# Optimization experiments

Measured on AMD Instinct MI355X. Metric: run time of the kernel, lower is better.

## Reference

```python
import jax, jax.numpy as jnp
import numpy as np


def crf_log_likelihood(logits, tags, mask, transitions, start_trans, end_trans):
    """AllenNLP-style linear-chain CRF log-likelihood, summed over the batch.
    logits: [B,T,K] float, tags: [B,T] int, mask: [B,T] float (1=valid).
    include_start_end_transitions=True.
    """
    B, T, K = logits.shape
    lt = jnp.transpose(logits, (1, 0, 2))          # [T,B,K]
    mt = jnp.transpose(mask, (1, 0))               # [T,B]
    tt = jnp.transpose(tags, (1, 0))               # [T,B]

    # ---- partition function (forward algorithm) ----
    alpha0 = start_trans + lt[0]                   # [B,K]

    def part_step(alpha, xs):
        emit, m = xs                               # emit [B,K], m [B]
        # inner[b,i,j] = alpha[b,i] + transitions[i,j] + emit[b,j]
        inner = alpha[:, :, None] + emit[:, None, :] + transitions[None, :, :]
        new_alpha = jax.nn.logsumexp(inner, axis=1)
        alpha = new_alpha * m[:, None] + alpha * (1.0 - m[:, None])
        return alpha, None

    alpha, _ = jax.lax.scan(part_step, alpha0, (lt[1:], mt[1:]))
    log_denominator = jax.nn.logsumexp(alpha + end_trans, axis=1)  # [B]

    # ---- joint (gold-path) score ----
    score0 = start_trans[tt[0]]                    # [B]

    def joint_step(score, xs):
        cur, nxt, emit, m_cur, m_nxt = xs
        trans_s = transitions[cur, nxt]                                   # [B]
        emit_s = jnp.take_along_axis(emit, cur[:, None], axis=1)[:, 0]    # [B]
        return score + trans_s * m_nxt + emit_s * m_cur, None

    score, _ = jax.lax.scan(joint_step, score0,
                            (tt[:-1], tt[1:], lt[:-1], mt[:-1], mt[1:]))
    last_idx = (jnp.sum(mt, axis=0) - 1.0).astype(jnp.int32)              # [B]
    last_tags = tt[last_idx, jnp.arange(B)]                               # [B]
    last_emit = jnp.take_along_axis(lt[-1], last_tags[:, None], axis=1)[:, 0]
    score = score + end_trans[last_tags] + last_emit * mt[-1]
    return jnp.sum(score - log_denominator)


def setup_inputs() -> dict:
    key = jax.random.key(0)
    ks = jax.random.split(key, 6)
    B, T, D, K = 64, 512, 768, 21
    vectors = jax.random.normal(ks[0], (B, T, D), dtype=jnp.float32)
    targets = jax.random.randint(ks[1], (B, T), 0, K, dtype=jnp.int32)
    mask = jnp.ones((B, T), dtype=jnp.int32)
    # Linear(input_dim, n_classes)
    W = jax.random.normal(ks[2], (K, D), dtype=jnp.float32) * (1.0 / np.sqrt(D))
    b = jax.random.normal(ks[3], (K,), dtype=jnp.float32) * 0.01
    transitions = jax.random.normal(ks[4], (K, K), dtype=jnp.float32) * 0.1
    se = jax.random.normal(ks[5], (2, K), dtype=jnp.float32) * 0.1
    return {"vectors": vectors, "targets": targets, "mask": mask,
            "W": W, "b": b, "transitions": transitions,
            "start_trans": se[0], "end_trans": se[1]}


def reference(vectors, targets, mask, W, b, transitions, start_trans, end_trans):
    logits = jnp.einsum('btd,kd->btk', vectors, W) + b     # proj
    maskf = mask.astype(logits.dtype)
    ll = crf_log_likelihood(logits, targets, maskf, transitions, start_trans, end_trans)
    loss = -ll / jnp.sum(maskf)
    return loss, logits
```

## Files before the change

### kernel.cpp

```cpp
#include <hip/hip_runtime.h>

#define B_ 64
#define T_ 512
#define D_ 768
#define K_ 21
#define NCHUNK 32
#define CLEN 16
#define GSTRIDE 448
#define LOG21 3.0445224377234229965f
#define WSTRIDE 776

using f16x8 = __attribute__((ext_vector_type(8))) _Float16;
using h16x4 = __attribute__((ext_vector_type(4))) _Float16;
using f32x4 = __attribute__((ext_vector_type(4))) float;

__global__ __launch_bounds__(256, 4) void proj_kernel(
    const float* __restrict__ A,
    const float* __restrict__ W,
    const float* __restrict__ bias,
    float* __restrict__ out)
{
    __shared__ _Float16 Wh[K_ * WSTRIDE];
    const int tid  = threadIdx.x;
    const int lane = tid & 63;
    const int w    = tid >> 6;
    const int m    = lane & 15;
    const int quad = lane >> 4;
    const int gw   = blockIdx.x * 4 + w;
    const float* Arow = A + ((size_t)gw * 16 + m) * D_;

    float4 pf[8];
    #pragma unroll
    for (int j = 0; j < 8; ++j) {
        const int s = j >> 1;
        const int off = s * 32 + quad * 8 + (j & 1) * 4;
        pf[j] = *(const float4*)(Arow + off);
    }

    {
        const float4* Wg = (const float4*)W;
        for (int i = tid; i < K_ * D_ / 4; i += 256) {
            const float4 v = Wg[i];
            const int fi = i * 4;
            const int r = fi / D_;
            const int c = fi - r * D_;
            h16x4 h;
            h[0] = (_Float16)v.x; h[1] = (_Float16)v.y;
            h[2] = (_Float16)v.z; h[3] = (_Float16)v.w;
            *(h16x4*)(&Wh[r * WSTRIDE + c]) = h;
        }
    }
    __syncthreads();

    f32x4 acc0 = {0.f, 0.f, 0.f, 0.f};
    f32x4 acc1 = {0.f, 0.f, 0.f, 0.f};
    const int n1 = (16 + m < K_) ? 16 + m : K_ - 1;

    for (int kt = 0; kt < 6; ++kt) {
        f16x8 af[4];
        #pragma unroll
        for (int s = 0; s < 4; ++s) {
            const float4 v0 = pf[2 * s], v1 = pf[2 * s + 1];
            f16x8 a;
            a[0] = (_Float16)v0.x; a[1] = (_Float16)v0.y;
            a[2] = (_Float16)v0.z; a[3] = (_Float16)v0.w;
            a[4] = (_Float16)v1.x; a[5] = (_Float16)v1.y;
            a[6] = (_Float16)v1.z; a[7] = (_Float16)v1.w;
            af[s] = a;
        }
        if (kt < 5) {
            const float* An = Arow + (kt + 1) * 128;
            #pragma unroll
            for (int j = 0; j < 8; ++j) {
                const int s = j >> 1;
                const int off = s * 32 + quad * 8 + (j & 1) * 4;
                pf[j] = *(const float4*)(An + off);
            }
        }
        #pragma unroll
        for (int s = 0; s < 4; ++s) {
            const f16x8 bf = *(const f16x8*)(&Wh[m  * WSTRIDE + kt * 128 + s * 32 + quad * 8]);
            const f16x8 cf = *(const f16x8*)(&Wh[n1 * WSTRIDE + kt * 128 + s * 32 + quad * 8]);
            acc0 = __builtin_amdgcn_mfma_f32_16x16x32_f16(af[s], bf, acc0, 0, 0, 0);
            acc1 = __builtin_amdgcn_mfma_f32_16x16x32_f16(af[s], cf, acc1, 0, 0, 0);
        }
    }

    const size_t rbase = (size_t)gw * 16 + quad * 4;
    {
        const float bb = bias[m];
        float* o = out + 1 + rbase * K_ + m;
        #pragma unroll
        for (int r = 0; r < 4; ++r) o[(size_t)r * K_] = acc0[r] + bb;
    }
    const int col2 = 16 + m;
    if (col2 < K_) {
        const float bb = bias[col2];
        float* o = out + 1 + rbase * K_ + col2;
        #pragma unroll
        for (int r = 0; r < 4; ++r) o[(size_t)r * K_] = acc1[r] + bb;
    }
}

__global__ __launch_bounds__(64, 1) void chunk_kernel(
    const float* __restrict__ outF,
    const int*   __restrict__ mask,
    const float* __restrict__ trans,
    float* __restrict__ G,
    float* __restrict__ SC,
    int*   __restrict__ cnt)
{
    __shared__ float M0[441], M1[441];
    __shared__ float sET[441];
    __shared__ float em[CLEN * K_];
    __shared__ float smx[CLEN];
    __shared__ int   smask[CLEN];

    const int c = blockIdx.x;
    const int b = blockIdx.y;
    const int lane = threadIdx.x;
    if (c == 0 && b == 0 && lane == 0) *cnt = 0;
    const int t0 = c * CLEN + 1;
    const int nst = min(CLEN, T_ - t0);
    const int i_ = lane / 3;
    const int jg = lane - i_ * 3;
    const bool act = lane < 63;

    const float* lg = outF + 1 + (size_t)b * T_ * K_;
    for (int idx = lane; idx < nst * K_; idx += 64) em[idx] = lg[t0 * K_ + idx];
    if (lane < nst) smask[lane] = mask[b * T_ + t0 + lane];
    for (int idx = lane; idx < 441; idx += 64) {
        M0[idx] = (idx % 22 == 0) ? 1.0f : 0.0f;
        sET[idx] = __expf(trans[idx]);
    }
    __syncthreads();

    if (lane < nst) {
        float mx = -1e30f;
        for (int j = 0; j < K_; ++j) mx = fmaxf(mx, em[lane * K_ + j]);
        smx[lane] = mx;
    }
    __syncthreads();
    for (int idx = lane; idx < nst * K_; idx += 64)
        em[idx] = __expf(em[idx] - smx[idx / K_]) * (1.0f / 21.0f);

    float ETc[K_ * 7];
    if (act) {
        #pragma unroll
        for (int mm = 0; mm < K_; ++mm) {
            #pragma unroll
            for (int q = 0; q < 7; ++q)
                ETc[mm * 7 + q] = sET[mm * K_ + jg * 7 + q];
        }
    }
    __syncthreads();

    int cur = 0;
    for (int s = 0; s < nst; ++s) {
        if (smask[s] != 0) {
            const float* Mr = cur ? M1 : M0;
            float*       Mw = cur ? M0 : M1;
            float facc[7] = {0.f,0.f,0.f,0.f,0.f,0.f,0.f};
            if (act) {
                #pragma unroll
                for (int mm = 0; mm < K_; ++mm) {
                    const float lm = Mr[i_ * K_ + mm];
                    #pragma unroll
                    for (int q = 0; q < 7; ++q)
                        facc[q] = fmaf(lm, ETc[mm * 7 + q], facc[q]);
                }
            }
            __syncthreads();
            if (act) {
                #pragma unroll
                for (int q = 0; q < 7; ++q)
                    Mw[i_ * K_ + jg * 7 + q] = facc[q] * em[s * K_ + jg * 7 + q];
            }
            __syncthreads();
            cur ^= 1;
        }
    }

    float* Gc = G + (size_t)(b * NCHUNK + c) * GSTRIDE;
    const float* Mf = cur ? M1 : M0;
    for (int idx = lane; idx < 441; idx += 64) Gc[idx] = Mf[idx];
    if (lane == 0) {
        float sc = 0.0f;
        for (int s = 0; s < nst; ++s)
            if (smask[s] != 0) sc += smx[s] + LOG21;
        SC[b * NCHUNK + c] = sc;
    }
}

__global__ __launch_bounds__(256) void scan_fin_kernel(
    const float* __restrict__ outF,
    const int*   __restrict__ tags,
    const int*   __restrict__ mask,
    const float* __restrict__ trans,
    const float* __restrict__ startT,
    const float* __restrict__ endT,
    const float* __restrict__ G,
    const float* __restrict__ SC,
    float* __restrict__ ll,
    float* __restrict__ msum,
    int*   __restrict__ cnt,
    float* __restrict__ outW)
{
    __shared__ float sG[NCHUNK * GSTRIDE];
    __shared__ float sm[T_];
    __shared__ int   st[T_];
    __shared__ float part[8];
    __shared__ int   lastF;
    const int tid = threadIdx.x;
    const int lane = tid & 63;
    const int w = tid >> 6;
    const int b = blockIdx.x;
    const float* lg = outF + 1 + (size_t)b * T_ * K_;

    {
        const float4* Gf4 = (const float4*)(G + (size_t)b * NCHUNK * GSTRIDE);
        float4* dst = (float4*)sG;
        for (int i = tid; i < NCHUNK * GSTRIDE / 4; i += 256) dst[i] = Gf4[i];
    }
    for (int t = tid; t < T_; t += 256) {
        sm[t] = (float)mask[b * T_ + t];
        st[t] = tags[b * T_ + t];
    }
    __syncthreads();

    float logZ = 0.0f;
    if (w == 0) {
        const float scv = (lane < NCHUNK) ? SC[b * NCHUNK + lane] : 0.0f;
        const int jc = min(lane, K_ - 1);
        float v = (lane < K_) ? __expf(startT[lane] + lg[lane]) : 0.0f;
        float C = 0.0f;
        for (int c = 0; c < NCHUNK; ++c) {
            const float* Gc = sG + c * GSTRIDE;
            float a0 = 0.f, a1 = 0.f, a2 = 0.f;
            #pragma unroll
            for (int i = 0; i < K_; i += 3) {
                a0 = fmaf(__shfl(v, i,     64), Gc[i * K_ + jc],       a0);
                a1 = fmaf(__shfl(v, i + 1, 64), Gc[(i + 1) * K_ + jc], a1);
                a2 = fmaf(__shfl(v, i + 2, 64), Gc[(i + 2) * K_ + jc], a2);
            }
            const float s = a0 + a1 + a2;
            const float s0 = __shfl(s, 0, 64);
            v = s / s0;
            C += __logf(s0) + __shfl(scv, c, 64);
        }
        float term = (lane < K_) ? v * __expf(endT[lane]) : 0.0f;
        #pragma unroll
        for (int off = 16; off >= 1; off >>= 1) term += __shfl_xor(term, off, 64);
        term += __shfl_xor(term, 32, 64);
        logZ = C + __logf(term);
    } else {
        float sc = 0.0f, ms = 0.0f;
        for (int t = tid - 64; t < T_; t += 192) {
            const float mt = sm[t];
            ms += mt;
            if (t < T_ - 1) {
                const int ct = st[t], nt2 = st[t + 1];
                sc += trans[ct * K_ + nt2] * sm[t + 1] + lg[t * K_ + ct] * mt;
            }
        }
        #pragma unroll
        for (int off = 32; off >= 1; off >>= 1) {
            sc += __shfl_xor(sc, off, 64);
            ms += __shfl_xor(ms, off, 64);
        }
        if (lane == 0) { part[w] = sc; part[4 + w] = ms; }
    }
    __syncthreads();

    if (tid == 0) {
        float sc = part[1] + part[2] + part[3];
        float ms = part[5] + part[6] + part[7];
        const int lastIdx = (int)ms - 1;
        const int lastTag = st[lastIdx];
        sc += startT[st[0]] + endT[lastTag] + lg[(T_ - 1) * K_ + lastTag] * sm[T_ - 1];
        ll[b]   = sc - logZ;
        msum[b] = ms;
        __threadfence();
        lastF = (atomicAdd(cnt, 1) == B_ - 1) ? 1 : 0;
    }
    __syncthreads();

    if (lastF != 0 && w == 0) {
        __threadfence();
        float l  = ll[lane];
        float mm = msum[lane];
        #pragma unroll
        for (int off = 32; off >= 1; off >>= 1) {
            l  += __shfl_xor(l,  off, 64);
            mm += __shfl_xor(mm, off, 64);
        }
        if (lane == 0) outW[0] = -l / mm;
    }
}

__global__ __launch_bounds__(64) void fin_kernel(
    const float* __restrict__ ll, const float* __restrict__ msum,
    float* __restrict__ outF)
{
    const int lane = threadIdx.x;
    float l = ll[lane];
    float m = msum[lane];
    #pragma unroll
    for (int off = 32; off >= 1; off >>= 1) {
        l += __shfl_xor(l, off, 64);
        m += __shfl_xor(m, off, 64);
    }
    if (lane == 0) outF[0] = -l / m;
}

__global__ __launch_bounds__(64) void crf_kernel(
    const float* __restrict__ outF,
    const int*   __restrict__ tags,
    const int*   __restrict__ mask,
    const float* __restrict__ trans,
    const float* __restrict__ startT,
    const float* __restrict__ endT,
    float* __restrict__ ws)
{
    __shared__ float se[T_ * K_];
    __shared__ float sm[T_];
    __shared__ int   st[T_];
    const int b = blockIdx.x;
    const int lane = threadIdx.x;

    const float* lg = outF + 1 + (size_t)b * T_ * K_;
    for (int i = lane; i < T_ * K_; i += 64) se[i] = lg[i];
    for (int t = lane; t < T_; t += 64) {
        sm[t] = (float)mask[b * T_ + t];
        st[t] = tags[b * T_ + t];
    }
    __syncthreads();

    const int jc = lane < K_ ? lane : K_ - 1;
    float ET[K_];
    #pragma unroll
    for (int i = 0; i < K_; ++i) ET[i] = __expf(trans[i * K_ + jc]);

    float a0   = startT[jc] + se[jc];
    float r0   = __shfl(a0, 0, 64);
    float aRel = a0 - r0;
    float C    = r0;

    for (int t = 1; t < T_; ++t) {
        if (sm[t] != 0.0f) {
            float e = __expf(aRel);
            float s = 0.0f;
            #pragma unroll
            for (int i = 0; i < K_; ++i)
                s = fmaf(__shfl(e, i, 64), ET[i], s);
            float raw = __logf(s) + se[t * K_ + jc];
            float rr  = __shfl(raw, 0, 64);
            aRel = raw - rr;
            C   += rr;
        }
    }

    float contrib = (lane < K_) ? __expf(aRel + endT[jc]) : 0.0f;
    #pragma unroll
    for (int off = 32; off >= 1; off >>= 1) contrib += __shfl_xor(contrib, off, 64);
    const float logZ = C + __logf(contrib);

    float sc = 0.0f, ms = 0.0f;
    for (int t = lane; t < T_; t += 64) {
        const float mt = sm[t];
        ms += mt;
        if (t < T_ - 1) {
            const int ct = st[t], nt2 = st[t + 1];
            sc += trans[ct * K_ + nt2] * sm[t + 1] + se[t * K_ + ct] * mt;
        }
    }
    #pragma unroll
    for (int off = 32; off >= 1; off >>= 1) {
        sc += __shfl_xor(sc, off, 64);
        ms += __shfl_xor(ms, off, 64);
    }
    if (lane == 0) {
        const int lastIdx = (int)ms - 1;
        const int lastTag = st[lastIdx];
        sc += startT[st[0]] + endT[lastTag] + se[(T_ - 1) * K_ + lastTag] * sm[T_ - 1];
        ws[b]      = sc - logZ;
        ws[B_ + b] = ms;
    }
}

extern "C" void kernel_launch(void* const* d_in, const int* in_sizes, int n_in,
                              void* d_out, int out_size, void* d_ws, size_t ws_size,
                              hipStream_t stream) {
    const float* A     = (const float*)d_in[0];
    const int*   tags  = (const int*)  d_in[1];
    const int*   mask  = (const int*)  d_in[2];
    const float* W     = (const float*)d_in[3];
    const float* bias  = (const float*)d_in[4];
    const float* trans = (const float*)d_in[5];
    const float* stT   = (const float*)d_in[6];
    const float* enT   = (const float*)d_in[7];
    float* outF = (float*)d_out;
    float* ws   = (float*)d_ws;

    const size_t gFloats = (size_t)B_ * NCHUNK * GSTRIDE;
    const size_t scOff   = gFloats;
    const size_t llOff   = scOff + (size_t)B_ * NCHUNK;
    const size_t msOff   = llOff + B_;
    const size_t cntOff  = msOff + B_;
    const size_t needBytes = cntOff * sizeof(float) + sizeof(int);

    proj_kernel<<<512, 256, 0, stream>>>(A, W, bias, outF);

    if (ws_size >= needBytes) {
        float* G   = ws;
        float* SC  = ws + scOff;
        float* llp = ws + llOff;
        float* msv = ws + msOff;
        int*   cnt = (int*)(ws + cntOff);
        chunk_kernel<<<dim3(NCHUNK, B_), 64, 0, stream>>>(outF, mask, trans, G, SC, cnt);
        scan_fin_kernel<<<B_, 256, 0, stream>>>(outF, tags, mask, trans, stT, enT, G, SC, llp, msv, cnt, outF);
    } else {
        crf_kernel<<<B_, 64, 0, stream>>>(outF, tags, mask, trans, stT, enT, ws);
        fin_kernel<<<1, 64, 0, stream>>>(ws, ws + B_, outF);
    }
}
```

Baseline: 209.5 us.

## Split projection K dimension across waves with LDS reduction

The projection kernel now has each block handle one 16-row tile, with the four waves each covering a 192-wide slice of the 768-deep reduction instead of each wave owning its own tile. Partial MFMA accumulators are summed through shared memory by wave 0, and the grid grows from 512 to 2048 blocks. The aim is more parallelism and all A loads issued up front, giving more memory-level parallelism on the bandwidth-bound read of the activations. The cost is that every block still converts the full W into fp16 in LDS, so that work is repeated four times as often, plus extra barriers and a reduction step.

```diff
diff --git a/kernel.cpp b/kernel.cpp
--- a/kernel.cpp
+++ b/kernel.cpp
@@ -26,12 +26,12 @@
     const int w    = tid >> 6;
     const int m    = lane & 15;
     const int quad = lane >> 4;
-    const int gw   = blockIdx.x * 4 + w;
-    const float* Arow = A + ((size_t)gw * 16 + m) * D_;
-
-    float4 pf[8];
-    #pragma unroll
-    for (int j = 0; j < 8; ++j) {
+    const int gw   = blockIdx.x;
+    const float* Arow = A + ((size_t)gw * 16 + m) * D_ + w * 192;
+
+    float4 pf[12];
+    #pragma unroll
+    for (int j = 0; j < 12; ++j) {
         const int s = j >> 1;
         const int off = s * 32 + quad * 8 + (j & 1) * 4;
         pf[j] = *(const float4*)(Arow + off);
@@ -55,50 +55,53 @@
     f32x4 acc0 = {0.f, 0.f, 0.f, 0.f};
     f32x4 acc1 = {0.f, 0.f, 0.f, 0.f};
     const int n1 = (16 + m < K_) ? 16 + m : K_ - 1;
-
-    for (int kt = 0; kt < 6; ++kt) {
-        f16x8 af[4];
-        #pragma unroll
-        for (int s = 0; s < 4; ++s) {
-            const float4 v0 = pf[2 * s], v1 = pf[2 * s + 1];
-            f16x8 a;
-            a[0] = (_Float16)v0.x; a[1] = (_Float16)v0.y;
-            a[2] = (_Float16)v0.z; a[3] = (_Float16)v0.w;
-            a[4] = (_Float16)v1.x; a[5] = (_Float16)v1.y;
-            a[6] = (_Float16)v1.z; a[7] = (_Float16)v1.w;
-            af[s] = a;
-        }
-        if (kt < 5) {
-            const float* An = Arow + (kt + 1) * 128;
+    const int kb = w * 192;
+
+    #pragma unroll
+    for (int s = 0; s < 6; ++s) {
+        const float4 v0 = pf[2 * s], v1 = pf[2 * s + 1];
+        f16x8 a;
+        a[0] = (_Float16)v0.x; a[1] = (_Float16)v0.y;
+        a[2] = (_Float16)v0.z; a[3] = (_Float16)v0.w;
+        a[4] = (_Float16)v1.x; a[5] = (_Float16)v1.y;
+        a[6] = (_Float16)v1.z; a[7] = (_Float16)v1.w;
+        const f16x8 bf = *(const f16x8*)(&Wh[m  * WSTRIDE + kb + s * 32 + quad * 8]);
+        const f16x8 cf = *(const f16x8*)(&Wh[n1 * WSTRIDE + kb + s * 32 + quad * 8]);
+        acc0 = __builtin_amdgcn_mfma_f32_16x16x32_f16(a, bf, acc0, 0, 0, 0);
+        acc1 = __builtin_amdgcn_mfma_f32_16x16x32_f16(a, cf, acc1, 0, 0, 0);
+    }
+
+    __syncthreads();
+    float* red = reinterpret_cast<float*>(&Wh[0]);
+    {
+        float* rw = red + (w * 8) * 64 + lane;
+        #pragma unroll
+        for (int r = 0; r < 4; ++r) {
+            rw[r * 64]       = acc0[r];
+            rw[(4 + r) * 64] = acc1[r];
+        }
+    }
+    __syncthreads();
+
+    if (w == 0) {
+        const size_t rbase = (size_t)gw * 16 + quad * 4;
+        const float bb0 = bias[m];
+        #pragma unroll
+        for (int r = 0; r < 4; ++r) {
+            const float s0 = red[(0 * 8 + r) * 64 + lane] + red[(1 * 8 + r) * 64 + lane]
+                           + red[(2 * 8 + r) * 64 + lane] + red[(3 * 8 + r) * 64 + lane];
+            out[1 + (rbase + r) * K_ + m] = s0 + bb0;
+        }
+        const int col2 = 16 + m;
+        if (col2 < K_) {
+            const float bb1 = bias[col2];
             #pragma unroll
-            for (int j = 0; j < 8; ++j) {
-                const int s = j >> 1;
-                const int off = s * 32 + quad * 8 + (j & 1) * 4;
-                pf[j] = *(const float4*)(An + off);
+            for (int r = 0; r < 4; ++r) {
+                const float s1 = red[(0 * 8 + 4 + r) * 64 + lane] + red[(1 * 8 + 4 + r) * 64 + lane]
+                               + red[(2 * 8 + 4 + r) * 64 + lane] + red[(3 * 8 + 4 + r) * 64 + lane];
+                out[1 + (rbase + r) * K_ + col2] = s1 + bb1;
             }
         }
-        #pragma unroll
-        for (int s = 0; s < 4; ++s) {
-            const f16x8 bf = *(const f16x8*)(&Wh[m  * WSTRIDE + kt * 128 + s * 32 + quad * 8]);
-            const f16x8 cf = *(const f16x8*)(&Wh[n1 * WSTRIDE + kt * 128 + s * 32 + quad * 8]);
-            acc0 = __builtin_amdgcn_mfma_f32_16x16x32_f16(af[s], bf, acc0, 0, 0, 0);
-            acc1 = __builtin_amdgcn_mfma_f32_16x16x32_f16(af[s], cf, acc1, 0, 0, 0);
-        }
-    }
-
-    const size_t rbase = (size_t)gw * 16 + quad * 4;
-    {
-        const float bb = bias[m];
-        float* o = out + 1 + rbase * K_ + m;
-        #pragma unroll
-        for (int r = 0; r < 4; ++r) o[(size_t)r * K_] = acc0[r] + bb;
-    }
-    const int col2 = 16 + m;
-    if (col2 < K_) {
-        const float bb = bias[col2];
-        float* o = out + 1 + rbase * K_ + col2;
-        #pragma unroll
-        for (int r = 0; r < 4; ++r) o[(size_t)r * K_] = acc1[r] + bb;
     }
 }
 
@@ -409,7 +412,7 @@
     const size_t cntOff  = msOff + B_;
     const size_t needBytes = cntOff * sizeof(float) + sizeof(int);
 
-    proj_kernel<<<512, 256, 0, stream>>>(A, W, bias, outF);
+    proj_kernel<<<2048, 256, 0, stream>>>(A, W, bias, outF);
 
     if (ws_size >= needBytes) {
         float* G   = ws;
```

Result: no change. 205.7 us (-1.8%).
